# Optimization experiments

Measured on AMD Instinct MI355X. Metric: run time of the kernel, lower is better.

The kernel has to match this reference:

```python
import jax, jax.numpy as jnp
import numpy as np

D_MODEL = 512
N_HEADS = 8
D_K = 64
D_V = 64
FACTOR = 1  # Autoformer AutoCorrelation default


def setup_inputs() -> dict:
    key = jax.random.key(0)
    ks = jax.random.split(key, 7)
    B, L = 8, 2048
    Q = jax.random.normal(ks[0], (B, L, D_MODEL), dtype=jnp.float32)
    K = jax.random.normal(ks[1], (B, L, D_MODEL), dtype=jnp.float32)
    V = jax.random.normal(ks[2], (B, L, D_MODEL), dtype=jnp.float32)
    s = 1.0 / np.sqrt(D_MODEL)
    WQ = jax.random.normal(ks[3], (D_MODEL, N_HEADS * D_K), dtype=jnp.float32) * s
    WK = jax.random.normal(ks[4], (D_MODEL, N_HEADS * D_K), dtype=jnp.float32) * s
    WV = jax.random.normal(ks[5], (D_MODEL, N_HEADS * D_V), dtype=jnp.float32) * s
    Wfc = jax.random.normal(ks[6], (N_HEADS * D_V, D_MODEL), dtype=jnp.float32) * s
    return {"Q": Q, "K": K, "V": V, "WQ": WQ, "WK": WK, "WV": WV, "Wfc": Wfc}


def _autocorrelation(q, k, v):
    # q, k, v: [B, L, H, E] (Autoformer AutoCorrelation, training-mode agg)
    B, L, H, E = q.shape
    qf = jnp.fft.rfft(q.transpose(0, 2, 3, 1), axis=-1)  # [B,H,E,Lf]
    kf = jnp.fft.rfft(k.transpose(0, 2, 3, 1), axis=-1)
    corr = jnp.fft.irfft(qf * jnp.conj(kf), n=L, axis=-1)  # [B,H,E,L]
    vals = v.transpose(0, 2, 3, 1)  # [B,H,E,L]
    top_k = int(FACTOR * np.log(L))
    mean_value = corr.mean(axis=(1, 2))  # [B,L] mean over heads & channels
    _, index = jax.lax.top_k(mean_value.mean(axis=0), top_k)  # [top_k] shared delays
    weights = mean_value[:, index]  # [B, top_k]
    tmp_corr = jax.nn.softmax(weights, axis=-1)  # [B, top_k]
    # roll(vals, -index[i]) along time for each selected delay, fully vectorized
    gather_idx = (jnp.arange(L)[None, :] + index[:, None]) % L  # [top_k, L]
    rolled = vals[..., gather_idx]  # [B,H,E,top_k,L]
    agg = jnp.einsum('bhekl,bk->bhel', rolled, tmp_corr)  # [B,H,E,L]
    return agg.transpose(0, 3, 1, 2)  # [B,L,H,E]


def reference(Q, K, V, WQ, WK, WV, Wfc):
    B, L, _ = Q.shape
    q_s = (Q @ WQ).reshape(B, L, N_HEADS, D_K)
    k_s = (K @ WK).reshape(B, L, N_HEADS, D_K)
    v_s = (V @ WV).reshape(B, L, N_HEADS, D_V)
    context = _autocorrelation(q_s, k_s, v_s)  # [B,L,H,Dv]
    context = context.reshape(B, L, N_HEADS * D_V)
    return context @ Wfc  # [B,L,d_model]
```

## Files before the change

### kernel.cpp

```cpp
#include <hip/hip_runtime.h>
#include <math.h>

#define B_ 8
#define L_ 2048
#define D_ 512
#define LOG2L 11
#define TOPK 7
#define M_ (B_ * L_)

typedef __attribute__((ext_vector_type(8))) _Float16 half8;
typedef __attribute__((ext_vector_type(4))) _Float16 half4;
typedef __attribute__((ext_vector_type(4))) float f32x4;

__global__ __launch_bounds__(256) void convw_kernel(
    const float* __restrict__ W0, const float* __restrict__ W1,
    const float* __restrict__ W2, const float* __restrict__ W3,
    _Float16* __restrict__ T0, _Float16* __restrict__ T1,
    _Float16* __restrict__ T2, _Float16* __restrict__ T3)
{
  __shared__ float tile[64][65];
  const int t = (int)threadIdx.x;
  const int mat = (int)blockIdx.x >> 6;
  const int tb = (int)blockIdx.x & 63;
  const float* W = (mat == 0) ? W0 : (mat == 1) ? W1 : (mat == 2) ? W2 : W3;
  _Float16* Wt = (mat == 0) ? T0 : (mat == 1) ? T1 : (mat == 2) ? T2 : T3;
  const int k0 = (tb >> 3) * 64;
  const int n0 = (tb & 7) * 64;
#pragma unroll
  for (int i = 0; i < 4; ++i) {
    const int kl = (t >> 4) + i * 16;
    const float4 v = *reinterpret_cast<const float4*>(&W[(size_t)(k0 + kl) * D_ + n0 + (t & 15) * 4]);
    tile[kl][(t & 15) * 4 + 0] = v.x;
    tile[kl][(t & 15) * 4 + 1] = v.y;
    tile[kl][(t & 15) * 4 + 2] = v.z;
    tile[kl][(t & 15) * 4 + 3] = v.w;
  }
  __syncthreads();
  const int nl = t >> 2, q = t & 3;
  half8 h0, h1;
#pragma unroll
  for (int j = 0; j < 8; ++j) {
    h0[j] = (_Float16)tile[q * 16 + j][nl];
    h1[j] = (_Float16)tile[q * 16 + 8 + j][nl];
  }
  _Float16* dst = &Wt[(size_t)(n0 + nl) * D_ + k0 + q * 16];
  *reinterpret_cast<half8*>(dst) = h0;
  *reinterpret_cast<half8*>(dst + 8) = h1;
}

#define LDSTR 40
#define NWG 1024

template <int INBF, int OUTMODE>
__global__ __launch_bounds__(256) void gemm_f16_kernel(
    const float* __restrict__ Af, const _Float16* __restrict__ Ah,
    const _Float16* __restrict__ Wt,
    float* __restrict__ Cf, _Float16* __restrict__ Ch)
{
  __shared__ __align__(16) _Float16 sA[128 * LDSTR];
  __shared__ __align__(16) _Float16 sB[64 * LDSTR];

  const int bid = (int)blockIdx.x;
  const int wg = (bid & 7) * (NWG >> 3) + (bid >> 3);
  const int m0 = (wg >> 3) << 7;
  const int n0 = (wg & 7) << 6;

  const int tid = (int)threadIdx.x;
  const int lane = tid & 63, wave = tid >> 6;
  const int wr = (wave >> 1) << 6;
  const int wc = (wave & 1) << 5;

  const int srow = tid >> 1;
  const int sc0 = (tid & 1) << 4;
  const int brow = tid >> 2;
  const int bc0 = (tid & 3) << 3;

  f32x4 acc[4][2];
  const f32x4 zero = {0.f, 0.f, 0.f, 0.f};
#pragma unroll
  for (int i = 0; i < 4; ++i)
#pragma unroll
    for (int j = 0; j < 2; ++j) acc[i][j] = zero;

  const int fr = lane & 15;
  const int g8 = (lane >> 4) << 3;

  for (int k0 = 0; k0 < D_; k0 += 32) {
    half8 ha0, ha1, hb;
    if constexpr (INBF == 0) {
      const float* ap = Af + (size_t)(m0 + srow) * D_ + k0 + sc0;
      float tmp[16];
#pragma unroll
      for (int j = 0; j < 4; ++j) {
        const float4 v = *reinterpret_cast<const float4*>(ap + j * 4);
        tmp[j * 4 + 0] = v.x; tmp[j * 4 + 1] = v.y;
        tmp[j * 4 + 2] = v.z; tmp[j * 4 + 3] = v.w;
      }
#pragma unroll
      for (int j = 0; j < 8; ++j) { ha0[j] = (_Float16)tmp[j]; ha1[j] = (_Float16)tmp[8 + j]; }
    } else {
      const _Float16* ap = Ah + (size_t)(m0 + srow) * D_ + k0 + sc0;
      ha0 = *reinterpret_cast<const half8*>(ap);
      ha1 = *reinterpret_cast<const half8*>(ap + 8);
    }
    hb = *reinterpret_cast<const half8*>(Wt + (size_t)(n0 + brow) * D_ + k0 + bc0);

    __syncthreads();
    *reinterpret_cast<half8*>(&sA[srow * LDSTR + sc0]) = ha0;
    *reinterpret_cast<half8*>(&sA[srow * LDSTR + sc0 + 8]) = ha1;
    *reinterpret_cast<half8*>(&sB[brow * LDSTR + bc0]) = hb;
    __syncthreads();

    half8 afr[4], bfr[2];
#pragma unroll
    for (int i = 0; i < 4; ++i)
      afr[i] = *reinterpret_cast<const half8*>(&sA[(wr + i * 16 + fr) * LDSTR + g8]);
#pragma unroll
    for (int i = 0; i < 2; ++i)
      bfr[i] = *reinterpret_cast<const half8*>(&sB[(wc + i * 16 + fr) * LDSTR + g8]);
#pragma unroll
    for (int mi = 0; mi < 4; ++mi)
#pragma unroll
      for (int ni = 0; ni < 2; ++ni)
        acc[mi][ni] = __builtin_amdgcn_mfma_f32_16x16x32_f16(afr[mi], bfr[ni], acc[mi][ni], 0, 0, 0);
  }

  const int orow = (lane >> 4) << 2;
  const int ocol = lane & 15;
  if constexpr (OUTMODE == 0) {
#pragma unroll
    for (int mi = 0; mi < 4; ++mi)
#pragma unroll
      for (int ni = 0; ni < 2; ++ni)
#pragma unroll
        for (int r = 0; r < 4; ++r)
          Cf[(size_t)(m0 + wr + mi * 16 + orow + r) * D_ + n0 + wc + ni * 16 + ocol] = acc[mi][ni][r];
  } else if constexpr (OUTMODE == 2) {
#pragma unroll
    for (int mi = 0; mi < 4; ++mi)
#pragma unroll
      for (int ni = 0; ni < 2; ++ni)
#pragma unroll
        for (int r = 0; r < 4; ++r)
          Ch[(size_t)(m0 + wr + mi * 16 + orow + r) * D_ + n0 + wc + ni * 16 + ocol] = (_Float16)acc[mi][ni][r];
  } else {
#pragma unroll
    for (int ni = 0; ni < 2; ++ni) {
      const size_t nrow = (size_t)(n0 + wc + ni * 16 + ocol) * M_;
#pragma unroll
      for (int mi = 0; mi < 4; ++mi) {
        half4 hv;
        hv[0] = (_Float16)acc[mi][ni][0]; hv[1] = (_Float16)acc[mi][ni][1];
        hv[2] = (_Float16)acc[mi][ni][2]; hv[3] = (_Float16)acc[mi][ni][3];
        *reinterpret_cast<half4*>(&Ch[nrow + m0 + wr + mi * 16 + orow]) = hv;
      }
    }
  }
}

__device__ __forceinline__ int rev11(int x) {
  return (int)(__brev((unsigned)x) >> (32 - LOG2L));
}

#define DCHUNK 4
#define PADI(i) ((i) + ((i) >> 5))

#define BFLY(j0, j1, wr_, wi_) { \
  const float ar = xr[j0], ai = xi[j0], br = xr[j1], bi = xi[j1]; \
  xr[j0] = ar + br; xi[j0] = ai + bi; \
  const float tr = ar - br, ti = ai - bi; \
  xr[j1] = tr * (wr_) - ti * (wi_); \
  xi[j1] = tr * (wi_) + ti * (wr_); }

__global__ __launch_bounds__(256) void corr_fft_kernel(
    const _Float16* __restrict__ qT, const _Float16* __restrict__ kT,
    float* __restrict__ S)
{
  __shared__ float re[2112];
  __shared__ float im[2112];
  const int t = (int)threadIdx.x;
  const int blk = (int)blockIdx.x;
  const int b = blk >> 7;
  const int d0 = (blk & 127) * DCHUNK;
  const int u2 = t & 31, u3 = t & 3;

  float w2048r, w2048i, w256r, w256i, w32r, w32i;
  {
    float s_, c_;
    __sincosf(-6.283185307179586f * (float)t / 2048.f, &s_, &c_);
    w2048r = c_; w2048i = s_;
    __sincosf(-6.283185307179586f * (float)u2 / 256.f, &s_, &c_);
    w256r = c_; w256i = s_;
    __sincosf(-6.283185307179586f * (float)u3 / 32.f, &s_, &c_);
    w32r = c_; w32i = s_;
  }
  const float w1024r = w2048r * w2048r - w2048i * w2048i, w1024i = 2.f * w2048r * w2048i;
  const float w512r  = w1024r * w1024r - w1024i * w1024i, w512i  = 2.f * w1024r * w1024i;
  const float w128r  = w256r * w256r - w256i * w256i,     w128i  = 2.f * w256r * w256i;
  const float w64r   = w128r * w128r - w128i * w128i,     w64i   = 2.f * w128r * w128i;
  const float w16r   = w32r * w32r - w32i * w32i,         w16i   = 2.f * w32r * w32i;
  const float w8r    = w16r * w16r - w16i * w16i,         w8i    = 2.f * w16r * w16i;

  const float C_ = 0.70710678118654752f;
  const float W8R[4] = {1.f, C_, 0.f, -C_};
  const float W8I[4] = {0.f, -C_, -1.f, -C_};

  float pr[8] = {}, pi_[8] = {};

  for (int dc = 0; dc < DCHUNK; ++dc) {
    const int d = d0 + dc;
    const _Float16* qrow = qT + (size_t)d * M_ + (size_t)b * L_;
    const _Float16* krow = kT + (size_t)d * M_ + (size_t)b * L_;

    float xr[8], xi[8];
#pragma unroll
    for (int j = 0; j < 8; ++j) {
      xr[j] = (float)qrow[t + 256 * j];
      xi[j] = (float)krow[t + 256 * j];
    }

#pragma unroll
    for (int j = 0; j < 4; ++j) {
      const float wr_ = w2048r * W8R[j] - w2048i * W8I[j];
      const float wi_ = w2048r * W8I[j] + w2048i * W8R[j];
      BFLY(j, j + 4, wr_, wi_);
    }
#pragma unroll
    for (int base = 0; base < 8; base += 4) {
      BFLY(base + 0, base + 2, w1024r, w1024i);
      BFLY(base + 1, base + 3, w1024i, -w1024r);
    }
#pragma unroll
    for (int a = 0; a < 8; a += 2) BFLY(a, a + 1, w512r, w512i);

    __syncthreads();
#pragma unroll
    for (int j = 0; j < 8; ++j) {
      const int p = t + 256 * j;
      re[PADI(p)] = xr[j]; im[PADI(p)] = xi[j];
    }
    __syncthreads();
#pragma unroll
    for (int j = 0; j < 8; ++j) {
      const int p = ((t >> 5) << 8) + u2 + 32 * j;
      xr[j] = re[PADI(p)]; xi[j] = im[PADI(p)];
    }

#pragma unroll
    for (int j = 0; j < 4; ++j) {
      const float wr_ = w256r * W8R[j] - w256i * W8I[j];
      const float wi_ = w256r * W8I[j] + w256i * W8R[j];
      BFLY(j, j + 4, wr_, wi_);
    }
#pragma unroll
    for (int base = 0; base < 8; base += 4) {
      BFLY(base + 0, base + 2, w128r, w128i);
      BFLY(base + 1, base + 3, w128i, -w128r);
    }
#pragma unroll
    for (int a = 0; a < 8; a += 2) BFLY(a, a + 1, w64r, w64i);

    __syncthreads();
#pragma unroll
    for (int j = 0; j < 8; ++j) {
      const int p = ((t >> 5) << 8) + u2 + 32 * j;
      re[PADI(p)] = xr[j]; im[PADI(p)] = xi[j];
    }
    __syncthreads();
#pragma unroll
    for (int j = 0; j < 8; ++j) {
      const int p = ((t >> 2) << 5) + u3 + 4 * j;
      xr[j] = re[PADI(p)]; xi[j] = im[PADI(p)];
    }

#pragma unroll
    for (int j = 0; j < 4; ++j) {
      const float wr_ = w32r * W8R[j] - w32i * W8I[j];
      const float wi_ = w32r * W8I[j] + w32i * W8R[j];
      BFLY(j, j + 4, wr_, wi_);
    }
#pragma unroll
    for (int base = 0; base < 8; base += 4) {
      BFLY(base + 0, base + 2, w16r, w16i);
      BFLY(base + 1, base + 3, w16i, -w16r);
    }
#pragma unroll
    for (int a = 0; a < 8; a += 2) BFLY(a, a + 1, w8r, w8i);

    __syncthreads();
#pragma unroll
    for (int j = 0; j < 8; ++j) {
      const int p = ((t >> 2) << 5) + u3 + 4 * j;
      re[PADI(p)] = xr[j]; im[PADI(p)] = xi[j];
    }
    __syncthreads();
#pragma unroll
    for (int j = 0; j < 8; ++j) {
      const int p = 8 * t + j;
      xr[j] = re[PADI(p)]; xi[j] = im[PADI(p)];
    }

#pragma unroll
    for (int base = 0; base < 8; base += 4) {
      BFLY(base + 0, base + 2, 1.f, 0.f);
      BFLY(base + 1, base + 3, 0.f, -1.f);
    }
#pragma unroll
    for (int a = 0; a < 8; a += 2) BFLY(a, a + 1, 1.f, 0.f);

#pragma unroll
    for (int j = 0; j < 8; ++j) {
      const int p = 8 * t + j;
      re[PADI(p)] = xr[j]; im[PADI(p)] = xi[j];
    }
    __syncthreads();

#pragma unroll
    for (int i = 0; i < 8; ++i) {
      const int p = t + 256 * i;
      const int f = rev11(p);
      const int fm = (L_ - f) & (L_ - 1);
      const int pm = rev11(fm);
      const float Ar = re[PADI(p)],  Ai = im[PADI(p)];
      const float Br = re[PADI(pm)], Bi = -im[PADI(pm)];
      const float Qr = 0.5f * (Ar + Br), Qi = 0.5f * (Ai + Bi);
      const float Cr = 0.5f * (Ai - Bi), Ci = 0.5f * (Ar - Br);
      pr[i]  += Qr * Cr - Qi * Ci;
      pi_[i] += Qr * Ci + Qi * Cr;
    }
    if (dc + 1 < DCHUNK) __syncthreads();
  }

#pragma unroll
  for (int i = 0; i < 8; ++i) {
    const int p = t + 256 * i;
    const int f = rev11(p);
    if (f <= L_ / 2) {
      atomicAdd(&S[((size_t)b * L_ + p) * 2 + 0], pr[i]);
      atomicAdd(&S[((size_t)b * L_ + p) * 2 + 1], pi_[i]);
    }
  }
}

__global__ __launch_bounds__(256) void ifft_kernel(
    const float* __restrict__ S, float* __restrict__ mv)
{
  __shared__ float re[L_];
  __shared__ float im[L_];
  const int b = blockIdx.x;
  for (int p = (int)threadIdx.x; p < L_; p += 256) {
    const int f = rev11(p);
    float sr, si;
    if (f <= L_ / 2) {
      sr = S[((size_t)b * L_ + p) * 2 + 0];
      si = S[((size_t)b * L_ + p) * 2 + 1];
    } else {
      const int pm = rev11(L_ - f);
      sr = S[((size_t)b * L_ + pm) * 2 + 0];
      si = -S[((size_t)b * L_ + pm) * 2 + 1];
    }
    re[p] = sr; im[p] = si;
  }
  __syncthreads();
  for (int s = 1; s <= LOG2L; ++s) {
    const int half = 1 << (s - 1);
    for (int j = (int)threadIdx.x; j < (L_ >> 1); j += 256) {
      const int pos = j & (half - 1);
      const int i0 = ((j >> (s - 1)) << s) + pos;
      const int i1 = i0 + half;
      const float ang = 3.14159265358979323846f * (float)pos / (float)half;
      float wi, wr;
      __sincosf(ang, &wi, &wr);
      const float br = re[i1], bi = im[i1];
      const float tr = br * wr - bi * wi;
      const float ti = br * wi + bi * wr;
      const float ar = re[i0], ai = im[i0];
      re[i0] = ar + tr; im[i0] = ai + ti;
      re[i1] = ar - tr; im[i1] = ai - ti;
    }
    __syncthreads();
  }
  const float scale = 1.0f / ((float)D_ * (float)L_);
  for (int l = (int)threadIdx.x; l < L_; l += 256)
    mv[(size_t)b * L_ + l] = re[l] * scale;
}

__global__ __launch_bounds__(1024) void topk_kernel(
    const float* __restrict__ mv, int* __restrict__ idx, float* __restrict__ wts)
{
  __shared__ float vals[L_];
  __shared__ float wm[16];
  __shared__ int wi[16];
  __shared__ int chosen[TOPK];
  const int t = (int)threadIdx.x;
  const int lane = t & 63, wv = t >> 6;
  float s0 = 0.f, s1 = 0.f;
#pragma unroll
  for (int b = 0; b < B_; ++b) {
    s0 += mv[(size_t)b * L_ + t];
    s1 += mv[(size_t)b * L_ + t + 1024];
  }
  vals[t] = s0; vals[t + 1024] = s1;
  __syncthreads();
  for (int kk = 0; kk < TOPK; ++kk) {
    float v0 = vals[t]; int i0 = t;
    const float v1 = vals[t + 1024];
    if (v1 > v0) { v0 = v1; i0 = t + 1024; }
#pragma unroll
    for (int off = 32; off; off >>= 1) {
      const float ov = __shfl_xor(v0, off, 64);
      const int oi = __shfl_xor(i0, off, 64);
      if (ov > v0 || (ov == v0 && oi < i0)) { v0 = ov; i0 = oi; }
    }
    if (lane == 0) { wm[wv] = v0; wi[wv] = i0; }
    __syncthreads();
    if (t == 0) {
      float m = wm[0]; int mi = wi[0];
      for (int i2 = 1; i2 < 16; ++i2)
        if (wm[i2] > m || (wm[i2] == m && wi[i2] < mi)) { m = wm[i2]; mi = wi[i2]; }
      chosen[kk] = mi; idx[kk] = mi; vals[mi] = -1e30f;
    }
    __syncthreads();
  }
  if (t < B_) {
    float w[TOPK];
    float mx = -1e30f;
#pragma unroll
    for (int kk = 0; kk < TOPK; ++kk) {
      w[kk] = mv[(size_t)t * L_ + chosen[kk]];
      mx = fmaxf(mx, w[kk]);
    }
    float sum = 0.f;
#pragma unroll
    for (int kk = 0; kk < TOPK; ++kk) { w[kk] = __expf(w[kk] - mx); sum += w[kk]; }
    const float inv = 1.0f / sum;
#pragma unroll
    for (int kk = 0; kk < TOPK; ++kk) wts[t * TOPK + kk] = w[kk] * inv;
  }
}

__global__ __launch_bounds__(256) void context_kernel(
    const _Float16* __restrict__ v, const int* __restrict__ idx,
    const float* __restrict__ wts, _Float16* __restrict__ ctx)
{
  const int blk = (int)blockIdx.x;
  const int b = blk >> 9;
  const int l = ((blk & 511) << 2) + ((int)threadIdx.x >> 6);
  const int lane = (int)threadIdx.x & 63;
  float acc[8] = {};
#pragma unroll
  for (int kk = 0; kk < TOPK; ++kk) {
    const float w = wts[b * TOPK + kk];
    const int src = (l + idx[kk]) & (L_ - 1);
    const half8 x = *reinterpret_cast<const half8*>(v + ((size_t)(b << LOG2L) + src) * D_ + lane * 8);
#pragma unroll
    for (int j = 0; j < 8; ++j) acc[j] = fmaf(w, (float)x[j], acc[j]);
  }
  half8 o;
#pragma unroll
  for (int j = 0; j < 8; ++j) o[j] = (_Float16)acc[j];
  *reinterpret_cast<half8*>(ctx + ((size_t)(b << LOG2L) + l) * D_ + lane * 8) = o;
}

extern "C" void kernel_launch(void* const* d_in, const int* in_sizes, int n_in,
                              void* d_out, int out_size, void* d_ws, size_t ws_size,
                              hipStream_t stream)
{
  (void)in_sizes; (void)n_in; (void)out_size; (void)ws_size;
  const float* Q   = (const float*)d_in[0];
  const float* K   = (const float*)d_in[1];
  const float* V   = (const float*)d_in[2];
  const float* WQ  = (const float*)d_in[3];
  const float* WK  = (const float*)d_in[4];
  const float* WV  = (const float*)d_in[5];
  const float* Wfc = (const float*)d_in[6];
  float* out = (float*)d_out;

  char* ws = (char*)d_ws;
  const size_t sz_h   = (size_t)M_ * D_ * sizeof(_Float16);
  const size_t sz_w16 = (size_t)D_ * D_ * sizeof(_Float16);
  _Float16*  qT16  = (_Float16*)(ws);
  _Float16*  kT16  = (_Float16*)(ws + sz_h);
  _Float16*  vs16  = (_Float16*)(ws + 2 * sz_h);
  _Float16*  ctx16 = (_Float16*)(ws + 3 * sz_h);
  _Float16*  WQt   = (_Float16*)(ws + 4 * sz_h);
  _Float16*  WKt   = (_Float16*)(ws + 4 * sz_h + sz_w16);
  _Float16*  WVt   = (_Float16*)(ws + 4 * sz_h + 2 * sz_w16);
  _Float16*  Wfct  = (_Float16*)(ws + 4 * sz_h + 3 * sz_w16);
  float*     S     = (float*)(ws + 4 * sz_h + 4 * sz_w16);
  float*     mv    = (float*)((char*)S + (size_t)B_ * L_ * 2 * sizeof(float));
  int*       idx   = (int*)((char*)mv + (size_t)B_ * L_ * sizeof(float));
  float*     wts   = (float*)((char*)idx + 64);

  convw_kernel<<<256, 256, 0, stream>>>(WQ, WK, WV, Wfc, WQt, WKt, WVt, Wfct);
  hipMemsetAsync(S, 0, (size_t)B_ * L_ * 2 * sizeof(float), stream);

  gemm_f16_kernel<0, 3><<<NWG, 256, 0, stream>>>(Q, nullptr, WQt, nullptr, qT16);
  gemm_f16_kernel<0, 3><<<NWG, 256, 0, stream>>>(K, nullptr, WKt, nullptr, kT16);

  corr_fft_kernel<<<B_ * (D_ / DCHUNK), 256, 0, stream>>>(qT16, kT16, S);
  ifft_kernel<<<B_, 256, 0, stream>>>(S, mv);
  topk_kernel<<<1, 1024, 0, stream>>>(mv, idx, wts);

  gemm_f16_kernel<0, 2><<<NWG, 256, 0, stream>>>(V, nullptr, WVt, nullptr, vs16);
  context_kernel<<<4096, 256, 0, stream>>>(vs16, idx, wts, ctx16);
  gemm_f16_kernel<1, 0><<<NWG, 256, 0, stream>>>(nullptr, ctx16, Wfct, out, nullptr);
}
```

Before: 191.5 us.

## Transpose GEMM block tile to 64x128 and swizzle context-kernel block order

Each GEMM work-group now computes a 64-row by 128-column output tile instead of 128x64. The A tile (the fp32 activations, converted to fp16 on load) shrinks and the weight tile grows, so each activation element is reused across more output columns. The change also affects L2 reuse of the weight panels and how many work-groups cover each row panel. The context kernel's block index is remapped so that consecutive hardware blocks are spread across batches, in the same way the GEMM remaps its blocks, which is meant to balance L2/XCD locality.

```diff
diff --git a/kernel.cpp b/kernel.cpp
--- a/kernel.cpp
+++ b/kernel.cpp
@@ -57,71 +57,70 @@
     const _Float16* __restrict__ Wt,
     float* __restrict__ Cf, _Float16* __restrict__ Ch)
 {
-  __shared__ __align__(16) _Float16 sA[128 * LDSTR];
-  __shared__ __align__(16) _Float16 sB[64 * LDSTR];
+  __shared__ __align__(16) _Float16 sA[64 * LDSTR];
+  __shared__ __align__(16) _Float16 sB[128 * LDSTR];
 
   const int bid = (int)blockIdx.x;
   const int wg = (bid & 7) * (NWG >> 3) + (bid >> 3);
-  const int m0 = (wg >> 3) << 7;
-  const int n0 = (wg & 7) << 6;
+  const int m0 = (wg >> 2) << 6;
+  const int n0 = (wg & 3) << 7;
 
   const int tid = (int)threadIdx.x;
   const int lane = tid & 63, wave = tid >> 6;
-  const int wr = (wave >> 1) << 6;
-  const int wc = (wave & 1) << 5;
-
-  const int srow = tid >> 1;
-  const int sc0 = (tid & 1) << 4;
-  const int brow = tid >> 2;
-  const int bc0 = (tid & 3) << 3;
-
-  f32x4 acc[4][2];
+  const int wr = (wave >> 1) << 5;
+  const int wc = (wave & 1) << 6;
+
+  const int arow = tid >> 2;
+  const int ac0 = (tid & 3) << 3;
+  const int brow = tid >> 1;
+  const int bc0 = (tid & 1) << 4;
+
+  f32x4 acc[2][4];
   const f32x4 zero = {0.f, 0.f, 0.f, 0.f};
 #pragma unroll
-  for (int i = 0; i < 4; ++i)
-#pragma unroll
-    for (int j = 0; j < 2; ++j) acc[i][j] = zero;
+  for (int i = 0; i < 2; ++i)
+#pragma unroll
+    for (int j = 0; j < 4; ++j) acc[i][j] = zero;
 
   const int fr = lane & 15;
   const int g8 = (lane >> 4) << 3;
 
   for (int k0 = 0; k0 < D_; k0 += 32) {
-    half8 ha0, ha1, hb;
+    half8 ha, hb0, hb1;
     if constexpr (INBF == 0) {
-      const float* ap = Af + (size_t)(m0 + srow) * D_ + k0 + sc0;
-      float tmp[16];
-#pragma unroll
-      for (int j = 0; j < 4; ++j) {
-        const float4 v = *reinterpret_cast<const float4*>(ap + j * 4);
-        tmp[j * 4 + 0] = v.x; tmp[j * 4 + 1] = v.y;
-        tmp[j * 4 + 2] = v.z; tmp[j * 4 + 3] = v.w;
-      }
-#pragma unroll
-      for (int j = 0; j < 8; ++j) { ha0[j] = (_Float16)tmp[j]; ha1[j] = (_Float16)tmp[8 + j]; }
+      const float* ap = Af + (size_t)(m0 + arow) * D_ + k0 + ac0;
+      const float4 v0 = *reinterpret_cast<const float4*>(ap);
+      const float4 v1 = *reinterpret_cast<const float4*>(ap + 4);
+      ha[0] = (_Float16)v0.x; ha[1] = (_Float16)v0.y;
+      ha[2] = (_Float16)v0.z; ha[3] = (_Float16)v0.w;
+      ha[4] = (_Float16)v1.x; ha[5] = (_Float16)v1.y;
+      ha[6] = (_Float16)v1.z; ha[7] = (_Float16)v1.w;
     } else {
-      const _Float16* ap = Ah + (size_t)(m0 + srow) * D_ + k0 + sc0;
-      ha0 = *reinterpret_cast<const half8*>(ap);
-      ha1 = *reinterpret_cast<const half8*>(ap + 8);
-    }
-    hb = *reinterpret_cast<const half8*>(Wt + (size_t)(n0 + brow) * D_ + k0 + bc0);
-
-    __syncthreads();
-    *reinterpret_cast<half8*>(&sA[srow * LDSTR + sc0]) = ha0;
-    *reinterpret_cast<half8*>(&sA[srow * LDSTR + sc0 + 8]) = ha1;
-    *reinterpret_cast<half8*>(&sB[brow * LDSTR + bc0]) = hb;
-    __syncthreads();
-
-    half8 afr[4], bfr[2];
+      ha = *reinterpret_cast<const half8*>(Ah + (size_t)(m0 + arow) * D_ + k0 + ac0);
+    }
+    {
+      const _Float16* bp = Wt + (size_t)(n0 + brow) * D_ + k0 + bc0;
+      hb0 = *reinterpret_cast<const half8*>(bp);
+      hb1 = *reinterpret_cast<const half8*>(bp + 8);
+    }
+
+    __syncthreads();
+    *reinterpret_cast<half8*>(&sA[arow * LDSTR + ac0]) = ha;
+    *reinterpret_cast<half8*>(&sB[brow * LDSTR + bc0]) = hb0;
+    *reinterpret_cast<half8*>(&sB[brow * LDSTR + bc0 + 8]) = hb1;
+    __syncthreads();
+
+    half8 afr[2], bfr[4];
+#pragma unroll
+    for (int i = 0; i < 2; ++i)
+      afr[i] = *reinterpret_cast<const half8*>(&sA[(wr + i * 16 + fr) * LDSTR + g8]);
 #pragma unroll
     for (int i = 0; i < 4; ++i)
-      afr[i] = *reinterpret_cast<const half8*>(&sA[(wr + i * 16 + fr) * LDSTR + g8]);
-#pragma unroll
-    for (int i = 0; i < 2; ++i)
       bfr[i] = *reinterpret_cast<const half8*>(&sB[(wc + i * 16 + fr) * LDSTR + g8]);
 #pragma unroll
-    for (int mi = 0; mi < 4; ++mi)
-#pragma unroll
-      for (int ni = 0; ni < 2; ++ni)
+    for (int mi = 0; mi < 2; ++mi)
+#pragma unroll
+      for (int ni = 0; ni < 4; ++ni)
         acc[mi][ni] = __builtin_amdgcn_mfma_f32_16x16x32_f16(afr[mi], bfr[ni], acc[mi][ni], 0, 0, 0);
   }
 
@@ -129,26 +128,26 @@
   const int ocol = lane & 15;
   if constexpr (OUTMODE == 0) {
 #pragma unroll
-    for (int mi = 0; mi < 4; ++mi)
-#pragma unroll
-      for (int ni = 0; ni < 2; ++ni)
+    for (int mi = 0; mi < 2; ++mi)
+#pragma unroll
+      for (int ni = 0; ni < 4; ++ni)
 #pragma unroll
         for (int r = 0; r < 4; ++r)
           Cf[(size_t)(m0 + wr + mi * 16 + orow + r) * D_ + n0 + wc + ni * 16 + ocol] = acc[mi][ni][r];
   } else if constexpr (OUTMODE == 2) {
 #pragma unroll
-    for (int mi = 0; mi < 4; ++mi)
-#pragma unroll
-      for (int ni = 0; ni < 2; ++ni)
+    for (int mi = 0; mi < 2; ++mi)
+#pragma unroll
+      for (int ni = 0; ni < 4; ++ni)
 #pragma unroll
         for (int r = 0; r < 4; ++r)
           Ch[(size_t)(m0 + wr + mi * 16 + orow + r) * D_ + n0 + wc + ni * 16 + ocol] = (_Float16)acc[mi][ni][r];
   } else {
 #pragma unroll
-    for (int ni = 0; ni < 2; ++ni) {
+    for (int ni = 0; ni < 4; ++ni) {
       const size_t nrow = (size_t)(n0 + wc + ni * 16 + ocol) * M_;
 #pragma unroll
-      for (int mi = 0; mi < 4; ++mi) {
+      for (int mi = 0; mi < 2; ++mi) {
         half4 hv;
         hv[0] = (_Float16)acc[mi][ni][0]; hv[1] = (_Float16)acc[mi][ni][1];
         hv[2] = (_Float16)acc[mi][ni][2]; hv[3] = (_Float16)acc[mi][ni][3];
@@ -443,9 +442,10 @@
     const _Float16* __restrict__ v, const int* __restrict__ idx,
     const float* __restrict__ wts, _Float16* __restrict__ ctx)
 {
-  const int blk = (int)blockIdx.x;
-  const int b = blk >> 9;
-  const int l = ((blk & 511) << 2) + ((int)threadIdx.x >> 6);
+  const int raw = (int)blockIdx.x;
+  const int wg = (raw & 7) * 512 + (raw >> 3);
+  const int b = wg >> 9;
+  const int l = ((wg & 511) << 2) + ((int)threadIdx.x >> 6);
   const int lane = (int)threadIdx.x & 63;
   float acc[8] = {};
 #pragma unroll
```

Measured after the change: 177.1 us. -7.5%, faster.
